# Kernel optimization log

Hardware: AMD Instinct MI355X
Metric: run time of the kernel (lower is better)

## Reference

```python
import jax, jax.numpy as jnp
import numpy as np

B = 2048          # number of tables (real batch size)
C = 8             # columns per table
D = 768           # hidden size (BERT-base)
TEMP = 0.07       # hp.temp
NEG_FILL = -10.0


def setup_inputs() -> dict:
    key = jax.random.key(0)
    k1, k2, k3 = jax.random.split(key, 3)
    n = B * C
    z = jax.random.normal(k1, (2 * n, D), jnp.float32) * 0.05
    idx = jnp.repeat(jnp.arange(B, dtype=jnp.int32), C)  # contiguous segment ids, as torch.full per table
    query = jax.random.normal(k2, (D, 1), jnp.float32) * 0.05
    attn_temp = jnp.ones((), jnp.float32)
    W = jax.random.normal(k3, (D, D), jnp.float32) * 0.02
    b = jnp.zeros((D,), jnp.float32)
    return {"z": z, "ori_table_indices": idx, "aug_table_indices": idx,
            "query": query, "attn_temp": attn_temp, "W": W, "b": b}


def _attn_pool(z, idx, query, t):
    # scatter-softmax attention pooling over variable-size table segments
    scores = (z @ query)[:, 0] / t                               # [n]
    e = jnp.exp(scores - scores.max())
    denom = jax.ops.segment_sum(e, idx, num_segments=B)[idx]     # [n]
    w = e / (denom + 1e-8)
    return jax.ops.segment_sum(z * w[:, None], idx, num_segments=B)  # [B, D]


def reference(z, ori_table_indices, aug_table_indices, query, attn_temp, W, b):
    n = B * C
    z_ori, z_aug = z[:n], z[n:]
    gx = _attn_pool(z_ori, ori_table_indices, query, attn_temp) @ W.T + b  # [B, D]
    hx = _attn_pool(z_aug, aug_table_indices, query, attn_temp) @ W.T + b  # [B, D]
    f = jnp.concatenate([gx, hx], axis=0)                                  # [2B, D]
    f = f / jnp.linalg.norm(f, axis=1, keepdims=True)
    sim = f @ f.T                                                          # [2B, 2B]
    N = 2 * B
    lab = jnp.concatenate([jnp.arange(B), jnp.arange(B)])
    labels = lab[None, :] == lab[:, None]                                  # [N, N] bool
    potential_pos = (sim > 0.9) & (~labels)
    safe_neg = (~potential_pos) & (~labels)
    # remove diagonal via rotation gather (order of negatives is irrelevant: topk sorts)
    cols = (jnp.arange(N)[:, None] + jnp.arange(1, N)[None, :]) % N        # [N, N-1]
    sim_od = jnp.take_along_axis(sim, cols, axis=1)
    safe_od = jnp.take_along_axis(safe_neg, cols, axis=1)
    # each row's single positive is its paired view at column (i+B) mod N
    pos = jnp.take_along_axis(sim, ((jnp.arange(N) + B) % N)[:, None], axis=1)  # [N, 1]
    neg = jnp.where(safe_od, sim_od, NEG_FILL)
    # data-dependent k; static-shape topk via descending sort + column mask
    k = jnp.maximum(1, jnp.floor(0.5 * jnp.mean(jnp.sum(safe_od, axis=1).astype(jnp.float32))).astype(jnp.int32))
    sneg = -jnp.sort(-neg, axis=1)                                         # descending
    new_neg = jnp.where(jnp.arange(N - 1)[None, :] < k, sneg, NEG_FILL)
    logits = jnp.concatenate([pos, new_neg], axis=1) / TEMP                # [N, N]
    # cross-entropy with target class 0
    loss = jnp.mean(jax.nn.logsumexp(logits, axis=1) - logits[:, 0])
    return loss
```

## Files before the change

### kernel.cpp

```cpp
#include <hip/hip_runtime.h>
#include <hip/hip_bf16.h>
#include <math.h>

#define Bq   2048
#define Cq   8
#define Dq   768
#define NROW 16384
#define NTOT 32768
#define Nq   4096
#define TEMPq 0.07f
#define NKC  96

typedef __attribute__((ext_vector_type(8))) short bf16x8;
typedef __attribute__((ext_vector_type(4))) float f32x4;
typedef __attribute__((ext_vector_type(8))) _Float16 f16x8;

__device__ __hip_bfloat16 g_pooledb[(size_t)Nq * Dq];
__device__ __hip_bfloat16 g_Wb[(size_t)Dq * Dq];
__device__ unsigned short g_fb[(size_t)Nq * Dq];
__device__ short          g_fbt[(size_t)NKC * Nq * 8];
__device__ _Float16       g_simh[(size_t)Nq * Nq];
__device__ unsigned int   g_viol;

#define GLDS16(src, dst) __builtin_amdgcn_global_load_lds( \
    (const __attribute__((address_space(1))) void*)(src),  \
    (__attribute__((address_space(3))) void*)(dst), 16, 0, 0)

__global__ __launch_bounds__(256) void prep_kernel(const float* __restrict__ z,
                                                   const float* __restrict__ query,
                                                   const float* __restrict__ attn_temp,
                                                   const float* __restrict__ W,
                                                   float* __restrict__ out) {
    if (blockIdx.x >= 1024) {
        int i = (blockIdx.x - 1024) * 256 + threadIdx.x;
        if (i == 0) { g_viol = 0u; out[0] = 0.f; }
        float4 v = ((const float4*)W)[i];
        short4 o;
        o.x = ((__hip_bfloat16_raw)__float2bfloat16(v.x)).x;
        o.y = ((__hip_bfloat16_raw)__float2bfloat16(v.y)).x;
        o.z = ((__hip_bfloat16_raw)__float2bfloat16(v.z)).x;
        o.w = ((__hip_bfloat16_raw)__float2bfloat16(v.w)).x;
        ((short4*)g_Wb)[i] = o;
        return;
    }
    int seg  = (int)((blockIdx.x * blockDim.x + threadIdx.x) >> 6);
    int lane = threadIdx.x & 63;
    if (seg >= Nq) return;
    int half = seg >> 11;
    int b    = seg & 2047;
    int baseRow = half * NROW + b * Cq;
    float invt = 1.f / attn_temp[0];

    float4 q4[3];
#pragma unroll
    for (int j = 0; j < 3; ++j) q4[j] = *(const float4*)(query + j * 256 + lane * 4);

    float4 v4[Cq][3];
    float s[Cq];
#pragma unroll
    for (int c = 0; c < Cq; ++c) {
        const float* zr = z + (size_t)(baseRow + c) * Dq;
        float acc = 0.f;
#pragma unroll
        for (int j = 0; j < 3; ++j) {
            float4 vz = *(const float4*)(zr + j * 256 + lane * 4);
            v4[c][j] = vz;
            acc += vz.x * q4[j].x + vz.y * q4[j].y + vz.z * q4[j].z + vz.w * q4[j].w;
        }
#pragma unroll
        for (int o = 32; o > 0; o >>= 1) acc += __shfl_xor(acc, o, 64);
        s[c] = acc * invt;
    }
    float m = s[0];
#pragma unroll
    for (int c = 1; c < Cq; ++c) m = fmaxf(m, s[c]);
    float e[Cq], denom = 0.f;
#pragma unroll
    for (int c = 0; c < Cq; ++c) { e[c] = expf(s[c] - m); denom += e[c]; }
    float inv = 1.f / (denom + 1e-8f);
#pragma unroll
    for (int j = 0; j < 3; ++j) {
        float4 acc = {0.f, 0.f, 0.f, 0.f};
#pragma unroll
        for (int c = 0; c < Cq; ++c) {
            acc.x += v4[c][j].x * e[c];
            acc.y += v4[c][j].y * e[c];
            acc.z += v4[c][j].z * e[c];
            acc.w += v4[c][j].w * e[c];
        }
        short4 o;
        o.x = ((__hip_bfloat16_raw)__float2bfloat16(acc.x * inv)).x;
        o.y = ((__hip_bfloat16_raw)__float2bfloat16(acc.y * inv)).x;
        o.z = ((__hip_bfloat16_raw)__float2bfloat16(acc.z * inv)).x;
        o.w = ((__hip_bfloat16_raw)__float2bfloat16(acc.w * inv)).x;
        *(short4*)((short*)g_pooledb + (size_t)seg * Dq + j * 256 + lane * 4) = o;
    }
}

__global__ __launch_bounds__(256) void fw_mfma_kernel(const float* __restrict__ bias) {
    __shared__ short lA[64 * 32];
    __shared__ short lB[128 * 32];
    const int bm = blockIdx.y * 64;
    const int bn = blockIdx.x * 128;

    const int tid  = threadIdx.x;
    const int wave = tid >> 6, lane = tid & 63;
    const int wm = wave >> 1, wn = wave & 1;

    const short* A  = (const short*)g_pooledb;
    const short* Bt = (const short*)g_Wb;

    const int srow = lane >> 2;
    const int scol = (lane & 3) * 8;
    const int c0 = wave * 2, c1 = wave * 2 + 1;

    f32x4 acc[2][4];
#pragma unroll
    for (int m = 0; m < 2; ++m)
#pragma unroll
        for (int n = 0; n < 4; ++n) acc[m][n] = (f32x4){0.f, 0.f, 0.f, 0.f};

    for (int k0 = 0; k0 < Dq; k0 += 32) {
        GLDS16(A  + (size_t)(bm + wave * 16 + srow) * Dq + k0 + scol, lA + wave * 512);
        GLDS16(Bt + (size_t)(bn + c0 * 16 + srow) * Dq + k0 + scol, lB + c0 * 512);
        GLDS16(Bt + (size_t)(bn + c1 * 16 + srow) * Dq + k0 + scol, lB + c1 * 512);
        __syncthreads();

        bf16x8 af[2], bfr[4];
#pragma unroll
        for (int m = 0; m < 2; ++m) {
            int row = wm * 32 + m * 16 + (lane & 15);
            af[m] = *(const bf16x8*)(lA + row * 32 + (lane >> 4) * 8);
        }
#pragma unroll
        for (int n = 0; n < 4; ++n) {
            int row = wn * 64 + n * 16 + (lane & 15);
            bfr[n] = *(const bf16x8*)(lB + row * 32 + (lane >> 4) * 8);
        }
#pragma unroll
        for (int m = 0; m < 2; ++m)
#pragma unroll
            for (int n = 0; n < 4; ++n)
                acc[m][n] = __builtin_amdgcn_mfma_f32_16x16x32_bf16(af[m], bfr[n], acc[m][n], 0, 0, 0);
        __syncthreads();
    }

#pragma unroll
    for (int m = 0; m < 2; ++m) {
        int rowb = bm + wm * 32 + m * 16 + (lane >> 4) * 4;
#pragma unroll
        for (int n = 0; n < 4; ++n) {
            int col = bn + wn * 64 + n * 16 + (lane & 15);
            float bc = bias[col];
#pragma unroll
            for (int j = 0; j < 4; ++j)
                g_fb[(size_t)(rowb + j) * Dq + col] =
                    ((__hip_bfloat16_raw)__float2bfloat16(acc[m][n][j] + bc)).x;
        }
    }
}

__global__ __launch_bounds__(256) void normalize_kernel() {
    __shared__ short rowbuf[16][776];
    const int tid = threadIdx.x;
    const int wave = tid >> 6, lane = tid & 63;
    const int r0 = blockIdx.x * 16;

    for (int rr = wave; rr < 16; rr += 4) {
        int row = r0 + rr;
        const unsigned short* fr = g_fb + (size_t)row * Dq;
        float v[12];
        float ss = 0.f;
#pragma unroll
        for (int j = 0; j < 6; ++j) {
            ushort2 u2 = *(const ushort2*)(fr + j * 128 + lane * 2);
            float f0 = __bfloat162float(*(__hip_bfloat16*)&u2.x);
            float f1 = __bfloat162float(*(__hip_bfloat16*)&u2.y);
            v[j * 2]     = f0;
            v[j * 2 + 1] = f1;
            ss += f0 * f0 + f1 * f1;
        }
#pragma unroll
        for (int o = 32; o > 0; o >>= 1) ss += __shfl_xor(ss, o, 64);
        float rn = 1.f / sqrtf(ss);
#pragma unroll
        for (int j = 0; j < 6; ++j) {
            rowbuf[rr][j * 128 + lane * 2]     = ((__hip_bfloat16_raw)__float2bfloat16(v[j * 2] * rn)).x;
            rowbuf[rr][j * 128 + lane * 2 + 1] = ((__hip_bfloat16_raw)__float2bfloat16(v[j * 2 + 1] * rn)).x;
        }
    }
    __syncthreads();
#pragma unroll
    for (int i = 0; i < 6; ++i) {
        int idx = i * 256 + tid;
        int ch = idx >> 4;
        int r  = idx & 15;
        bf16x8 val = *(const bf16x8*)&rowbuf[r][ch * 8];
        *(bf16x8*)&g_fbt[((size_t)ch * Nq + r0 + r) * 8] = val;
    }
}

#define STAGE_SIM(b, kt_) do {                                                          \
    _Pragma("unroll")                                                                   \
    for (int i = 0; i < 4; ++i) {                                                       \
        GLDS16(fbt + ((size_t)((kt_) * 8 + wave) * Nq + bm + i * 64 + lane) * 8,        \
               As + ((b) * 2048 + wave * 256 + i * 64) * 8);                            \
        GLDS16(fbt + ((size_t)((kt_) * 8 + wave) * Nq + bn + i * 64 + lane) * 8,        \
               Bs + ((b) * 2048 + wave * 256 + i * 64) * 8);                            \
    }                                                                                   \
} while (0)

__global__ __launch_bounds__(512) void sim_mfma_kernel() {
    extern __shared__ short smem[];
    short* As = smem;
    short* Bs = smem + 32768;

    const int tid  = threadIdx.x;
    const int wave = tid >> 6, lane = tid & 63;
    const int wm = wave >> 2, wn = wave & 3;
    const int bm = blockIdx.y * 256, bn = blockIdx.x * 256;
    const short* fbt = g_fbt;

    f32x4 acc[8][4];
#pragma unroll
    for (int mi = 0; mi < 8; ++mi)
#pragma unroll
        for (int ni = 0; ni < 4; ++ni) acc[mi][ni] = (f32x4){0.f, 0.f, 0.f, 0.f};

    STAGE_SIM(0, 0);

#pragma unroll 1
    for (int kt = 0; kt < 12; ++kt) {
        const int cur = kt & 1;
        if (kt < 11) {
            STAGE_SIM(cur ^ 1, kt + 1);
            asm volatile("s_waitcnt vmcnt(8)" ::: "memory");
        } else {
            asm volatile("s_waitcnt vmcnt(0)" ::: "memory");
        }
        __builtin_amdgcn_s_barrier();
        __builtin_amdgcn_sched_barrier(0);

#pragma unroll
        for (int ks = 0; ks < 2; ++ks) {
            bf16x8 af[8], bfr[4];
            const int kc = (ks * 4 + (lane >> 4)) * 256;
#pragma unroll
            for (int mi = 0; mi < 8; ++mi)
                af[mi] = *(const bf16x8*)(As + (cur * 2048 + kc + wm * 128 + mi * 16 + (lane & 15)) * 8);
#pragma unroll
            for (int ni = 0; ni < 4; ++ni)
                bfr[ni] = *(const bf16x8*)(Bs + (cur * 2048 + kc + wn * 64 + ni * 16 + (lane & 15)) * 8);
            __builtin_amdgcn_s_setprio(1);
#pragma unroll
            for (int mi = 0; mi < 8; ++mi)
#pragma unroll
                for (int ni = 0; ni < 4; ++ni)
                    acc[mi][ni] = __builtin_amdgcn_mfma_f32_16x16x32_bf16(af[mi], bfr[ni], acc[mi][ni], 0, 0, 0);
            __builtin_amdgcn_s_setprio(0);
        }
        __builtin_amdgcn_sched_barrier(0);
        __builtin_amdgcn_s_barrier();
    }

    int vio = 0;
#pragma unroll
    for (int mi = 0; mi < 8; ++mi) {
        int rowb = bm + wm * 128 + mi * 16 + (lane >> 4) * 4;
#pragma unroll
        for (int ni = 0; ni < 4; ++ni) {
            int col = bn + wn * 64 + ni * 16 + (lane & 15);
#pragma unroll
            for (int j = 0; j < 4; ++j) {
                float x = acc[mi][ni][j];
                g_simh[(size_t)(rowb + j) * Nq + col] = (_Float16)x;
                vio += (x > 0.9f) && ((((rowb + j) ^ col) & 2047) != 0);
            }
        }
    }
#pragma unroll
    for (int o = 32; o > 0; o >>= 1) vio += __shfl_xor(vio, o, 64);
    if (lane == 0 && vio > 0) atomicAdd(&g_viol, (unsigned int)vio);
}

__global__ __launch_bounds__(256) void lse_kernel(float* __restrict__ out) {
    const int tid = threadIdx.x;
    const int wave = tid >> 6, lane = tid & 63;
    const int row_id = blockIdx.x * 4 + wave;
    const _Float16* row = g_simh + (size_t)row_id * Nq;
    const int labi = row_id & 2047;
    const float invT = 1.0f / TEMPq;

    long long total = (long long)Nq * 4094LL - (long long)g_viol;
    int k = (int)(total / 8192LL);
    if (k < 1) k = 1;

    float v[64];
    float mx = -1e30f, mn = 1e30f;
    int cnt = 0;
#pragma unroll
    for (int q = 0; q < 8; ++q) {
        int j0 = q * 512 + lane * 8;
        f16x8 x8 = *(const f16x8*)(row + j0);
#pragma unroll
        for (int s = 0; s < 8; ++s) {
            int jj = q * 8 + s;
            int j  = j0 + s;
            float xv = (float)x8[s];
            bool sf = (xv <= 0.9f) && (((j ^ labi) & 2047) != 0);
            float val = sf ? xv : -2.0f;
            v[jj] = val;
            mx = fmaxf(mx, val);
            mn = fminf(mn, sf ? xv : 2.0f);
            cnt += (int)__popcll(__ballot(sf));
        }
    }
#pragma unroll
    for (int o = 32; o > 0; o >>= 1) {
        mx = fmaxf(mx, __shfl_xor(mx, o, 64));
        mn = fminf(mn, __shfl_xor(mn, o, 64));
    }

    const float pos = (float)row[(row_id + Bq) & (Nq - 1)];
    const float mxs = (cnt > 0) ? mx : -10.0f;
    const float ml  = fmaxf(pos, mxs) * invT;

    float lo = mn - 1e-3f, hi = mx;
    int c_hi = 0;
    const bool need = (cnt > k);
    if (need) {
        for (int it = 0; it < 12; ++it) {
            float mid = 0.5f * (lo + hi);
            int c = 0;
#pragma unroll
            for (int jj = 0; jj < 64; ++jj)
                c += (int)__popcll(__ballot(v[jj] > mid));
            if (c > k) lo = mid; else { hi = mid; c_hi = c; }
        }
    }

    float shi = 0.f, st = 0.f; int nt = 0;
#pragma unroll
    for (int jj = 0; jj < 64; ++jj) {
        float x = v[jj];
        float ev = __expf(x * invT - ml);
        if (!need)       { if (x > -1.5f) shi += ev; }
        else if (x > hi) { shi += ev; }
        else if (x > lo) { st += ev; nt++; }
    }
#pragma unroll
    for (int o = 32; o > 0; o >>= 1) {
        shi += __shfl_xor(shi, o, 64);
        st  += __shfl_xor(st,  o, 64);
        nt  += __shfl_xor(nt,  o, 64);
    }
    __shared__ float sblk[4];
    if (lane == 0) {
        float S = __expf(pos * invT - ml) + shi;
        if (need && c_hi < k && nt > 0)
            S += st * (float)(k - c_hi) / (float)nt;
        sblk[wave] = (logf(S) + ml) - pos * invT;
    }
    __syncthreads();
    if (tid == 0) {
        float bs = (sblk[0] + sblk[1] + sblk[2] + sblk[3]) * (1.0f / (float)Nq);
        atomicAdd(out, bs);
    }
}

extern "C" void kernel_launch(void* const* d_in, const int* in_sizes, int n_in,
                              void* d_out, int out_size, void* d_ws, size_t ws_size,
                              hipStream_t stream) {
    const float* z         = (const float*)d_in[0];
    const float* query     = (const float*)d_in[3];
    const float* attn_temp = (const float*)d_in[4];
    const float* W         = (const float*)d_in[5];
    const float* bias      = (const float*)d_in[6];
    float* out = (float*)d_out;

    prep_kernel<<<1024 + (Dq * Dq / 4) / 256, 256, 0, stream>>>(z, query, attn_temp, W, out);
    fw_mfma_kernel<<<dim3(Dq / 128, Nq / 64), 256, 0, stream>>>(bias);
    normalize_kernel<<<Nq / 16, 256, 0, stream>>>();
    sim_mfma_kernel<<<dim3(16, 16), 512, 131072, stream>>>();
    lse_kernel<<<Nq / 4, 256, 0, stream>>>(out);
}
```

Before: 109.5 us.

## Fuse row normalization into projection and similarity epilogues, drop normalize kernel

The projection GEMM epilogue now stages its tile in shared memory, writes it directly into the transposed bf16 layout used by the similarity GEMM, and accumulates per-row squared norms into a global buffer with atomics. The similarity epilogue applies the reciprocal row and column norms to each dot product. This removes the separate normalize kernel launch and the round trip through the intermediate feature buffer. In exchange, the similarity GEMM now multiplies unnormalized bf16 features, so rounding differs slightly. The sum of squares is taken from fp32 values while the GEMM uses bf16 values, which adds small mismatches and float atomics add nondeterminism.

```diff
diff --git a/kernel.cpp b/kernel.cpp
--- a/kernel.cpp
+++ b/kernel.cpp
@@ -17,8 +17,8 @@
 
 __device__ __hip_bfloat16 g_pooledb[(size_t)Nq * Dq];
 __device__ __hip_bfloat16 g_Wb[(size_t)Dq * Dq];
-__device__ unsigned short g_fb[(size_t)Nq * Dq];
 __device__ short          g_fbt[(size_t)NKC * Nq * 8];
+__device__ float          g_ssum[Nq];
 __device__ _Float16       g_simh[(size_t)Nq * Nq];
 __device__ unsigned int   g_viol;
 
@@ -34,6 +34,10 @@
     if (blockIdx.x >= 1024) {
         int i = (blockIdx.x - 1024) * 256 + threadIdx.x;
         if (i == 0) { g_viol = 0u; out[0] = 0.f; }
+        if (blockIdx.x == 1024) {
+#pragma unroll
+            for (int q = 0; q < 16; ++q) g_ssum[threadIdx.x * 16 + q] = 0.f;
+        }
         float4 v = ((const float4*)W)[i];
         short4 o;
         o.x = ((__hip_bfloat16_raw)__float2bfloat16(v.x)).x;
@@ -100,6 +104,7 @@
 __global__ __launch_bounds__(256) void fw_mfma_kernel(const float* __restrict__ bias) {
     __shared__ short lA[64 * 32];
     __shared__ short lB[128 * 32];
+    __shared__ short ct[64][136];
     const int bm = blockIdx.y * 64;
     const int bn = blockIdx.x * 128;
 
@@ -145,58 +150,50 @@
         __syncthreads();
     }
 
+    float ssp[2][4];
+#pragma unroll
+    for (int m = 0; m < 2; ++m)
+#pragma unroll
+        for (int j = 0; j < 4; ++j) ssp[m][j] = 0.f;
 #pragma unroll
     for (int m = 0; m < 2; ++m) {
-        int rowb = bm + wm * 32 + m * 16 + (lane >> 4) * 4;
+        int rloc = wm * 32 + m * 16 + (lane >> 4) * 4;
 #pragma unroll
         for (int n = 0; n < 4; ++n) {
-            int col = bn + wn * 64 + n * 16 + (lane & 15);
-            float bc = bias[col];
+            int cloc = wn * 64 + n * 16 + (lane & 15);
+            float bc = bias[bn + cloc];
+#pragma unroll
+            for (int j = 0; j < 4; ++j) {
+                float x = acc[m][n][j] + bc;
+                ct[rloc + j][cloc] = ((__hip_bfloat16_raw)__float2bfloat16(x)).x;
+                ssp[m][j] += x * x;
+            }
+        }
+    }
+#pragma unroll
+    for (int m = 0; m < 2; ++m)
+#pragma unroll
+        for (int j = 0; j < 4; ++j) {
+#pragma unroll
+            for (int o = 1; o < 16; o <<= 1) ssp[m][j] += __shfl_xor(ssp[m][j], o, 64);
+        }
+    if ((lane & 15) == 0) {
+        int rbase = bm + wm * 32 + (lane >> 4) * 4;
+#pragma unroll
+        for (int m = 0; m < 2; ++m)
 #pragma unroll
             for (int j = 0; j < 4; ++j)
-                g_fb[(size_t)(rowb + j) * Dq + col] =
-                    ((__hip_bfloat16_raw)__float2bfloat16(acc[m][n][j] + bc)).x;
-        }
-    }
-}
-
-__global__ __launch_bounds__(256) void normalize_kernel() {
-    __shared__ short rowbuf[16][776];
-    const int tid = threadIdx.x;
-    const int wave = tid >> 6, lane = tid & 63;
-    const int r0 = blockIdx.x * 16;
-
-    for (int rr = wave; rr < 16; rr += 4) {
-        int row = r0 + rr;
-        const unsigned short* fr = g_fb + (size_t)row * Dq;
-        float v[12];
-        float ss = 0.f;
-#pragma unroll
-        for (int j = 0; j < 6; ++j) {
-            ushort2 u2 = *(const ushort2*)(fr + j * 128 + lane * 2);
-            float f0 = __bfloat162float(*(__hip_bfloat16*)&u2.x);
-            float f1 = __bfloat162float(*(__hip_bfloat16*)&u2.y);
-            v[j * 2]     = f0;
-            v[j * 2 + 1] = f1;
-            ss += f0 * f0 + f1 * f1;
-        }
-#pragma unroll
-        for (int o = 32; o > 0; o >>= 1) ss += __shfl_xor(ss, o, 64);
-        float rn = 1.f / sqrtf(ss);
-#pragma unroll
-        for (int j = 0; j < 6; ++j) {
-            rowbuf[rr][j * 128 + lane * 2]     = ((__hip_bfloat16_raw)__float2bfloat16(v[j * 2] * rn)).x;
-            rowbuf[rr][j * 128 + lane * 2 + 1] = ((__hip_bfloat16_raw)__float2bfloat16(v[j * 2 + 1] * rn)).x;
-        }
+                atomicAdd(&g_ssum[rbase + m * 16 + j], ssp[m][j]);
     }
     __syncthreads();
-#pragma unroll
-    for (int i = 0; i < 6; ++i) {
+
+#pragma unroll
+    for (int i = 0; i < 4; ++i) {
         int idx = i * 256 + tid;
-        int ch = idx >> 4;
-        int r  = idx & 15;
-        bf16x8 val = *(const bf16x8*)&rowbuf[r][ch * 8];
-        *(bf16x8*)&g_fbt[((size_t)ch * Nq + r0 + r) * 8] = val;
+        int r   = idx & 63;
+        int chl = idx >> 6;
+        bf16x8 val = *(const bf16x8*)&ct[r][chl * 8];
+        *(bf16x8*)&g_fbt[((size_t)(bn / 8 + chl) * Nq + bm + r) * 8] = val;
     }
 }
 
@@ -263,16 +260,25 @@
         __builtin_amdgcn_s_barrier();
     }
 
+    float rn_c[4];
+#pragma unroll
+    for (int ni = 0; ni < 4; ++ni) {
+        int col = bn + wn * 64 + ni * 16 + (lane & 15);
+        rn_c[ni] = rsqrtf(g_ssum[col]);
+    }
     int vio = 0;
 #pragma unroll
     for (int mi = 0; mi < 8; ++mi) {
         int rowb = bm + wm * 128 + mi * 16 + (lane >> 4) * 4;
+        float rn_r[4];
+#pragma unroll
+        for (int j = 0; j < 4; ++j) rn_r[j] = rsqrtf(g_ssum[rowb + j]);
 #pragma unroll
         for (int ni = 0; ni < 4; ++ni) {
             int col = bn + wn * 64 + ni * 16 + (lane & 15);
 #pragma unroll
             for (int j = 0; j < 4; ++j) {
-                float x = acc[mi][ni][j];
+                float x = acc[mi][ni][j] * rn_r[j] * rn_c[ni];
                 g_simh[(size_t)(rowb + j) * Nq + col] = (_Float16)x;
                 vio += (x > 0.9f) && ((((rowb + j) ^ col) & 2047) != 0);
             }
@@ -380,7 +386,6 @@
 
     prep_kernel<<<1024 + (Dq * Dq / 4) / 256, 256, 0, stream>>>(z, query, attn_temp, W, out);
     fw_mfma_kernel<<<dim3(Dq / 128, Nq / 64), 256, 0, stream>>>(bias);
-    normalize_kernel<<<Nq / 16, 256, 0, stream>>>();
     sim_mfma_kernel<<<dim3(16, 16), 512, 131072, stream>>>();
     lse_kernel<<<Nq / 4, 256, 0, stream>>>(out);
 }
```

New measurement: 106.3 us. 2.9% less time.
